# Performance work log

Measured on AMD Instinct MI355X. Metric: run time of the kernel, lower is better.

Reference implementation:

```python
import jax, jax.numpy as jnp
import numpy as np

N, E, D_IN, D_HID, D_OUT = 50000, 800000, 128, 128, 128


def setup_inputs() -> dict:
    key = jax.random.key(0)
    ks = jax.random.split(key, 10)
    x = jax.random.normal(ks[0], (N, D_IN), dtype=jnp.float32)
    edge_index = jax.random.randint(ks[1], (2, E), 0, N, dtype=jnp.int64)
    def xavier(k, fan_in, fan_out):
        lim = jnp.sqrt(6.0 / (fan_in + fan_out)).astype(jnp.float32)
        return jax.random.uniform(k, (fan_in, fan_out), jnp.float32, -lim, lim)
    return {
        "x": x,
        "edge_index": edge_index,
        "W1l": xavier(ks[2], D_IN, D_HID), "b1l": jnp.zeros((D_HID,), jnp.float32),
        "W1r": xavier(ks[3], D_IN, D_HID),
        "W2l": xavier(ks[4], D_HID, D_OUT), "b2l": jnp.zeros((D_OUT,), jnp.float32),
        "W2r": xavier(ks[5], D_HID, D_OUT),
        "Wfc": xavier(ks[6], D_OUT, 2), "bfc": jnp.zeros((2,), jnp.float32),
    }


def _mean_aggregate(x, src, dst, num_nodes):
    # gather neighbor (source) features, scatter-mean to destination nodes
    msgs = x[src]                                        # [E, D]
    summed = jax.ops.segment_sum(msgs, dst, num_segments=num_nodes)
    ones = jnp.ones((src.shape[0],), x.dtype)
    counts = jax.ops.segment_sum(ones, dst, num_segments=num_nodes)
    return summed / jnp.maximum(counts, 1.0)[:, None]


def _l2_normalize(x, eps=1e-12):
    # matches torch F.normalize(p=2, dim=-1): divide by clamp(norm, min=eps)
    norm = jnp.sqrt(jnp.sum(x * x, axis=-1, keepdims=True))
    return x / jnp.maximum(norm, eps)


def _sage_conv(x, src, dst, Wl, bl, Wr):
    agg = _mean_aggregate(x, src, dst, x.shape[0])
    out = agg @ Wl + bl + x @ Wr
    return _l2_normalize(out)


def reference(x, edge_index, W1l, b1l, W1r, W2l, b2l, W2r, Wfc, bfc):
    src, dst = edge_index[0], edge_index[1]  # PyG: row=source(j), col=target(i)
    h = _sage_conv(x, src, dst, W1l, b1l, W1r)
    h = jax.nn.relu(h)
    h = _sage_conv(h, src, dst, W2l, b2l, W2r)
    logits = h @ Wfc + bfc
    return jax.nn.softmax(logits, axis=-1)
```

## Files before the change

### kernel.cpp

```cpp
#include <hip/hip_runtime.h>

#define D 128
#define CBITS 8

typedef __attribute__((ext_vector_type(8))) short short8;
typedef __attribute__((ext_vector_type(4))) float f32x4;

__device__ __forceinline__ unsigned short f2b(float f) {
    unsigned u = __builtin_bit_cast(unsigned, f);
    u += 0x7fffu + ((u >> 16) & 1u);
    return (unsigned short)(u >> 16);
}
__device__ __forceinline__ float b2f(unsigned short b) {
    unsigned u = ((unsigned)b) << 16;
    return __builtin_bit_cast(float, u);
}


__global__ __launch_bounds__(256) void prep_kernel(
    const float* __restrict__ x, unsigned short* __restrict__ acat, int nCast, int n8,
    const float* __restrict__ W1l, const float* __restrict__ W1r,
    const float* __restrict__ W2l, const float* __restrict__ W2r,
    unsigned short* __restrict__ WT1, unsigned short* __restrict__ WT2,
    int4* __restrict__ zeroPtr, int* __restrict__ offsets, int nnodes, int E) {
    const int b = blockIdx.x;
    if (b < nCast) {
        int g = b * 256 + threadIdx.x;
        if (g < n8) {
            int row = g >> 4, chunk = g & 15;
            const float4 v0 = *reinterpret_cast<const float4*>(x + (size_t)g * 8);
            const float4 v1 = *reinterpret_cast<const float4*>(x + (size_t)g * 8 + 4);
            short8 r;
            r[0] = (short)f2b(v0.x); r[1] = (short)f2b(v0.y); r[2] = (short)f2b(v0.z); r[3] = (short)f2b(v0.w);
            r[4] = (short)f2b(v1.x); r[5] = (short)f2b(v1.y); r[6] = (short)f2b(v1.z); r[7] = (short)f2b(v1.w);
            *reinterpret_cast<short8*>(acat + (size_t)row * 256 + 128 + chunk * 8) = r;
        }
    } else if (b < nCast + 256) {
        int bb = b - nCast;
        int layer = bb >> 7;
        int j = bb & 127;
        int k = threadIdx.x;
        const float* Wl = layer ? W2l : W1l;
        const float* Wr = layer ? W2r : W1r;
        unsigned short* WT = layer ? WT2 : WT1;
        float v = (k < 128) ? Wl[k * D + j] : Wr[(k - 128) * D + j];
        WT[(size_t)j * 256 + k] = f2b(v);
    } else {
        if (threadIdx.x < 128) zeroPtr[threadIdx.x] = make_int4(0, 0, 0, 0);
        if (threadIdx.x == 0) offsets[nnodes] = E;
    }
}


__global__ __launch_bounds__(256) void bucket_count_kernel(
    const int* __restrict__ dst, int* __restrict__ bucketCnt, int E) {
    __shared__ int hist[256];
    const int t = threadIdx.x;
    hist[t] = 0;
    __syncthreads();
    const int base = blockIdx.x * 4096;
#pragma unroll
    for (int i = 0; i < 16; ++i) {
        int e = base + i * 256 + t;
        if (e < E) atomicAdd(&hist[dst[e] >> CBITS], 1);
    }
    __syncthreads();
    if (hist[t]) atomicAdd(&bucketCnt[t], hist[t]);
}

__global__ __launch_bounds__(256) void bin_coarse_kernel(
    const int* __restrict__ src, const int* __restrict__ dst,
    const int* __restrict__ bucketCnt, int* __restrict__ cursorA,
    int2* __restrict__ staging, int E) {

    __shared__ int hist[256];
    __shared__ int lcur[256];
    const int t = threadIdx.x;

    int cnt = bucketCnt[t];
    lcur[t] = cnt;
    __syncthreads();
    for (int d = 1; d < 256; d <<= 1) {
        int u = (t >= d) ? lcur[t - d] : 0;
        __syncthreads();
        lcur[t] += u;
        __syncthreads();
    }
    const int myBase = lcur[t] - cnt;
    __syncthreads();

    hist[t] = 0;
    __syncthreads();

    const int base = blockIdx.x * 4096;
    int sreg[16], dreg[16];
#pragma unroll
    for (int i = 0; i < 16; ++i) {
        int e = base + i * 256 + t;
        int s = 0, d = -1;
        if (e < E) {
            s = src[e]; d = dst[e];
            atomicAdd(&hist[d >> CBITS], 1);
        }
        sreg[i] = s; dreg[i] = d;
    }
    __syncthreads();
    {
        int h = hist[t];
        lcur[t] = myBase + (h ? atomicAdd(&cursorA[t], h) : 0);
    }
    __syncthreads();
#pragma unroll
    for (int i = 0; i < 16; ++i) {
        if (dreg[i] >= 0) {
            int p = atomicAdd(&lcur[dreg[i] >> CBITS], 1);
            staging[p] = make_int2(sreg[i], dreg[i]);
        }
    }
}

__global__ __launch_bounds__(256) void bucket_build_kernel(
    const int2* __restrict__ staging, const int* __restrict__ bucketCnt,
    int* __restrict__ offsets, int* __restrict__ csr, int nnodes) {

    __shared__ int A1[256];
    __shared__ int A2[256];
    const int t = threadIdx.x;
    const int b = blockIdx.x;

    int cnt = bucketCnt[t];
    A1[t] = cnt;
    __syncthreads();
    for (int d = 1; d < 256; d <<= 1) {
        int u = (t >= d) ? A1[t - d] : 0;
        __syncthreads();
        A1[t] += u;
        __syncthreads();
    }
    const int end  = A1[b];
    const int base = end - bucketCnt[b];
    __syncthreads();

    A1[t] = 0;
    __syncthreads();
    for (int i = base + t; i < end; i += 256)
        atomicAdd(&A1[staging[i].y & ((1 << CBITS) - 1)], 1);
    __syncthreads();
    A2[t] = A1[t];
    __syncthreads();
    for (int d = 1; d < 256; d <<= 1) {
        int u = (t >= d) ? A2[t - d] : 0;
        __syncthreads();
        A2[t] += u;
        __syncthreads();
    }
    const int excl = A2[t] - A1[t];
    const int node = (b << CBITS) + t;
    if (node < nnodes) offsets[node] = base + excl;
    __syncthreads();
    A1[t] = base + excl;
    __syncthreads();
    for (int i = base + t; i < end; i += 256) {
        int2 sd = staging[i];
        int p = atomicAdd(&A1[sd.y & ((1 << CBITS) - 1)], 1);
        csr[p] = sd.x;
    }
}


__global__ __launch_bounds__(256) void aggregate_kernel(
    const unsigned short* __restrict__ xin,
    const int* __restrict__ offsets, const int* __restrict__ csr,
    unsigned short* __restrict__ out,
    int nnodes) {
    int node = blockIdx.x * 16 + (threadIdx.x >> 4);
    int l16 = threadIdx.x & 15;
    if (node >= nnodes) return;
    int lo = offsets[node], hi = offsets[node + 1];
    float acc[8] = {0.f, 0.f, 0.f, 0.f, 0.f, 0.f, 0.f, 0.f};
    int k = lo;
    for (; k + 8 <= hi; k += 8) {
        int s[8];
        short8 v[8];
#pragma unroll
        for (int u = 0; u < 8; ++u) s[u] = csr[k + u];
#pragma unroll
        for (int u = 0; u < 8; ++u)
            v[u] = *reinterpret_cast<const short8*>(xin + (size_t)s[u] * 256 + l16 * 8);
#pragma unroll
        for (int u = 0; u < 8; ++u)
#pragma unroll
            for (int i = 0; i < 8; ++i) acc[i] += b2f((unsigned short)v[u][i]);
    }
    for (; k < hi; ++k) {
        int s = csr[k];
        const short8 v = *reinterpret_cast<const short8*>(xin + (size_t)s * 256 + l16 * 8);
#pragma unroll
        for (int i = 0; i < 8; ++i) acc[i] += b2f((unsigned short)v[i]);
    }
    float inv = 1.0f / fmaxf((float)(hi - lo), 1.0f);
    short8 r;
#pragma unroll
    for (int i = 0; i < 8; ++i) r[i] = (short)f2b(acc[i] * inv);
    *reinterpret_cast<short8*>(out + (size_t)node * 256 + l16 * 8) = r;
}


template <bool RELU, bool HEAD>
__global__ __launch_bounds__(256) void sage_mfma_kernel(
    const unsigned short* __restrict__ Acat, const unsigned short* __restrict__ WT,
    const float* __restrict__ bias, unsigned short* __restrict__ hout, int out_stride,
    const float* __restrict__ Wfc, const float* __restrict__ bfc,
    float* __restrict__ outf, int nnodes) {

    __shared__ unsigned short Blds[128 * 256];
    const int tid = threadIdx.x;

    {
        const short8* wsrc = reinterpret_cast<const short8*>(WT);
#pragma unroll
        for (int it = 0; it < 16; ++it) {
            int u = it * 256 + tid;
            int row = u >> 5, c = u & 31;
            int cs = c ^ (row & 7);
            *reinterpret_cast<short8*>(
                reinterpret_cast<char*>(Blds) + row * 512 + cs * 16) = wsrc[u];
        }
    }
    __syncthreads();

    const int w = tid >> 6, l = tid & 63;
    const int r16 = l & 15, g = l >> 4;
    const int rowbase = blockIdx.x * 128 + w * 32;

    f32x4 acc[2][8];
#pragma unroll
    for (int j = 0; j < 8; ++j) {
        float bj = bias[j * 16 + r16];
        acc[0][j] = (f32x4){bj, bj, bj, bj};
        acc[1][j] = (f32x4){bj, bj, bj, bj};
    }

    const unsigned short* ap0 = Acat + (size_t)(rowbase + r16) * 256 + g * 8;
    const unsigned short* ap1 = ap0 + 16 * 256;

#pragma unroll
    for (int ks = 0; ks < 8; ++ks) {
        const short8 a0 = *reinterpret_cast<const short8*>(ap0 + ks * 32);
        const short8 a1 = *reinterpret_cast<const short8*>(ap1 + ks * 32);
        const int cs = ((ks * 4 + g) ^ (r16 & 7)) * 16;
#pragma unroll
        for (int j = 0; j < 8; ++j) {
            const short8 b = *reinterpret_cast<const short8*>(
                reinterpret_cast<const char*>(Blds) + (j * 16 + r16) * 512 + cs);
            acc[0][j] = __builtin_amdgcn_mfma_f32_16x16x32_bf16(a0, b, acc[0][j], 0, 0, 0);
            acc[1][j] = __builtin_amdgcn_mfma_f32_16x16x32_bf16(a1, b, acc[1][j], 0, 0, 0);
        }
    }

#pragma unroll
    for (int rb = 0; rb < 2; ++rb) {
        float ss[4] = {0.f, 0.f, 0.f, 0.f};
#pragma unroll
        for (int j = 0; j < 8; ++j)
#pragma unroll
            for (int i = 0; i < 4; ++i) ss[i] += acc[rb][j][i] * acc[rb][j][i];
#pragma unroll
        for (int m = 1; m < 16; m <<= 1)
#pragma unroll
            for (int i = 0; i < 4; ++i) ss[i] += __shfl_xor(ss[i], m, 64);

        if (!HEAD) {
#pragma unroll
            for (int i = 0; i < 4; ++i) {
                int row = rowbase + rb * 16 + g * 4 + i;
                if (row >= nnodes) continue;
                float sc = 1.0f / fmaxf(sqrtf(ss[i]), 1e-12f);
#pragma unroll
                for (int j = 0; j < 8; ++j) {
                    float v = acc[rb][j][i] * sc;
                    if (RELU) v = fmaxf(v, 0.f);
                    hout[(size_t)row * out_stride + j * 16 + r16] = f2b(v);
                }
            }
        } else {
            float w0[8], w1[8];
#pragma unroll
            for (int j = 0; j < 8; ++j) {
                const float2 wv = *reinterpret_cast<const float2*>(Wfc + (j * 16 + r16) * 2);
                w0[j] = wv.x; w1[j] = wv.y;
            }
            const float b0 = bfc[0], b1 = bfc[1];
#pragma unroll
            for (int i = 0; i < 4; ++i) {
                float sc = 1.0f / fmaxf(sqrtf(ss[i]), 1e-12f);
                float l0 = 0.f, l1 = 0.f;
#pragma unroll
                for (int j = 0; j < 8; ++j) {
                    float v = acc[rb][j][i] * sc;
                    l0 = fmaf(v, w0[j], l0);
                    l1 = fmaf(v, w1[j], l1);
                }
#pragma unroll
                for (int m = 1; m < 16; m <<= 1) {
                    l0 += __shfl_xor(l0, m, 64);
                    l1 += __shfl_xor(l1, m, 64);
                }
                int row = rowbase + rb * 16 + g * 4 + i;
                if (r16 == 0 && row < nnodes) {
                    float d0 = l0 + b0, d1 = l1 + b1;
                    float mx = fmaxf(d0, d1);
                    float e0 = expf(d0 - mx), e1 = expf(d1 - mx);
                    float inv = 1.0f / (e0 + e1);
                    outf[(size_t)row * 2]     = e0 * inv;
                    outf[(size_t)row * 2 + 1] = e1 * inv;
                }
            }
        }
    }
}


extern "C" void kernel_launch(void* const* d_in, const int* in_sizes, int n_in,
                              void* d_out, int out_size, void* d_ws, size_t ws_size,
                              hipStream_t stream) {
    const float* x   = (const float*)d_in[0];
    const int*   ei  = (const int*)d_in[1];
    const float* W1l = (const float*)d_in[2];
    const float* b1l = (const float*)d_in[3];
    const float* W1r = (const float*)d_in[4];
    const float* W2l = (const float*)d_in[5];
    const float* b2l = (const float*)d_in[6];
    const float* W2r = (const float*)d_in[7];
    const float* Wfc = (const float*)d_in[8];
    const float* bfc = (const float*)d_in[9];

    const int N = in_sizes[0] / D;
    const int E = in_sizes[1] / 2;
    const int* src = ei;
    const int* dst = ei + E;
    const int NBC = (N + (1 << CBITS) - 1) >> CBITS;

    unsigned short* Acat1 = (unsigned short*)d_ws;
    unsigned short* Acat2 = Acat1 + (size_t)N * 256;
    int2* staging         = (int2*)Acat2;
    unsigned short* WT1   = Acat2 + (size_t)N * 256;
    unsigned short* WT2   = WT1 + 128 * 256;
    int* bucketCnt  = (int*)(WT2 + 128 * 256);
    int* cursorA    = bucketCnt + 256;
    int* offsets    = cursorA + 256;
    int* csr        = offsets + N + 1;

    const int nCast = (N * 16 + 255) / 256;

    prep_kernel<<<nCast + 256 + 1, 256, 0, stream>>>(
        x, Acat1, nCast, N * 16, W1l, W1r, W2l, W2r, WT1, WT2,
        (int4*)bucketCnt, offsets, N, E);

    bucket_count_kernel<<<(E + 4095) / 4096, 256, 0, stream>>>(dst, bucketCnt, E);
    bin_coarse_kernel<<<(E + 4095) / 4096, 256, 0, stream>>>(src, dst, bucketCnt, cursorA, staging, E);
    bucket_build_kernel<<<NBC, 256, 0, stream>>>(staging, bucketCnt, offsets, csr, N);

    aggregate_kernel<<<(N + 15) / 16, 256, 0, stream>>>(Acat1 + 128, offsets, csr, Acat1, N);
    sage_mfma_kernel<true, false><<<(N + 127) / 128, 256, 0, stream>>>(
        Acat1, WT1, b1l, Acat2 + 128, 256, nullptr, nullptr, nullptr, N);

    aggregate_kernel<<<(N + 15) / 16, 256, 0, stream>>>(Acat2 + 128, offsets, csr, Acat2, N);
    sage_mfma_kernel<false, true><<<(N + 127) / 128, 256, 0, stream>>>(
        Acat2, WT2, b2l, nullptr, 0, Wfc, bfc, (float*)d_out, N);
}
```

Before: 133.3 us.

## Split aggregation into feature-column slabs and pack staging edges into one int

The aggregate kernel now splits the 128 features into four 32-column slabs handled by separate block groups. Each node is served by 4 lanes instead of 16, so a block covers 64 nodes. The point is that concurrently running blocks touch a smaller slice of the gathered rows, which should help L2 locality. Staging entries are also packed into a single int (16-bit source plus 8-bit local destination) instead of int2, halving staging traffic. The packing assumes node ids fit in 16 bits, but N is 50000, so this holds only for sizes up to 65535.

```diff
diff --git a/kernel.cpp b/kernel.cpp
--- a/kernel.cpp
+++ b/kernel.cpp
@@ -71,7 +71,7 @@
 __global__ __launch_bounds__(256) void bin_coarse_kernel(
     const int* __restrict__ src, const int* __restrict__ dst,
     const int* __restrict__ bucketCnt, int* __restrict__ cursorA,
-    int2* __restrict__ staging, int E) {
+    int* __restrict__ staging, int E) {
 
     __shared__ int hist[256];
     __shared__ int lcur[256];
@@ -114,13 +114,13 @@
     for (int i = 0; i < 16; ++i) {
         if (dreg[i] >= 0) {
             int p = atomicAdd(&lcur[dreg[i] >> CBITS], 1);
-            staging[p] = make_int2(sreg[i], dreg[i]);
+            staging[p] = sreg[i] | ((dreg[i] & 255) << 16);
         }
     }
 }
 
 __global__ __launch_bounds__(256) void bucket_build_kernel(
-    const int2* __restrict__ staging, const int* __restrict__ bucketCnt,
+    const int* __restrict__ staging, const int* __restrict__ bucketCnt,
     int* __restrict__ offsets, int* __restrict__ csr, int nnodes) {
 
     __shared__ int A1[256];
@@ -144,7 +144,7 @@
     A1[t] = 0;
     __syncthreads();
     for (int i = base + t; i < end; i += 256)
-        atomicAdd(&A1[staging[i].y & ((1 << CBITS) - 1)], 1);
+        atomicAdd(&A1[(staging[i] >> 16) & 255], 1);
     __syncthreads();
     A2[t] = A1[t];
     __syncthreads();
@@ -161,9 +161,9 @@
     A1[t] = base + excl;
     __syncthreads();
     for (int i = base + t; i < end; i += 256) {
-        int2 sd = staging[i];
-        int p = atomicAdd(&A1[sd.y & ((1 << CBITS) - 1)], 1);
-        csr[p] = sd.x;
+        int p = staging[i];
+        int c = atomicAdd(&A1[(p >> 16) & 255], 1);
+        csr[c] = p & 0xFFFF;
     }
 }
 
@@ -172,10 +172,14 @@
     const unsigned short* __restrict__ xin,
     const int* __restrict__ offsets, const int* __restrict__ csr,
     unsigned short* __restrict__ out,
-    int nnodes) {
-    int node = blockIdx.x * 16 + (threadIdx.x >> 4);
-    int l16 = threadIdx.x & 15;
+    int nnodes, int nodeBlocks) {
+    const int q  = blockIdx.x / nodeBlocks;
+    const int nb = blockIdx.x - q * nodeBlocks;
+    const int node = nb * 64 + (threadIdx.x >> 2);
+    const int l4 = threadIdx.x & 3;
     if (node >= nnodes) return;
+    const int coff = q * 32 + l4 * 8;
+    const unsigned short* xq = xin + coff;
     int lo = offsets[node], hi = offsets[node + 1];
     float acc[8] = {0.f, 0.f, 0.f, 0.f, 0.f, 0.f, 0.f, 0.f};
     int k = lo;
@@ -186,7 +190,7 @@
         for (int u = 0; u < 8; ++u) s[u] = csr[k + u];
 #pragma unroll
         for (int u = 0; u < 8; ++u)
-            v[u] = *reinterpret_cast<const short8*>(xin + (size_t)s[u] * 256 + l16 * 8);
+            v[u] = *reinterpret_cast<const short8*>(xq + (size_t)s[u] * 256);
 #pragma unroll
         for (int u = 0; u < 8; ++u)
 #pragma unroll
@@ -194,7 +198,7 @@
     }
     for (; k < hi; ++k) {
         int s = csr[k];
-        const short8 v = *reinterpret_cast<const short8*>(xin + (size_t)s * 256 + l16 * 8);
+        const short8 v = *reinterpret_cast<const short8*>(xq + (size_t)s * 256);
 #pragma unroll
         for (int i = 0; i < 8; ++i) acc[i] += b2f((unsigned short)v[i]);
     }
@@ -202,7 +206,7 @@
     short8 r;
 #pragma unroll
     for (int i = 0; i < 8; ++i) r[i] = (short)f2b(acc[i] * inv);
-    *reinterpret_cast<short8*>(out + (size_t)node * 256 + l16 * 8) = r;
+    *reinterpret_cast<short8*>(out + (size_t)node * 256 + coff) = r;
 }
 
 
@@ -343,7 +347,7 @@
 
     unsigned short* Acat1 = (unsigned short*)d_ws;
     unsigned short* Acat2 = Acat1 + (size_t)N * 256;
-    int2* staging         = (int2*)Acat2;
+    int* staging          = (int*)Acat2;
     unsigned short* WT1   = Acat2 + (size_t)N * 256;
     unsigned short* WT2   = WT1 + 128 * 256;
     int* bucketCnt  = (int*)(WT2 + 128 * 256);
@@ -352,6 +356,7 @@
     int* csr        = offsets + N + 1;
 
     const int nCast = (N * 16 + 255) / 256;
+    const int nodeBlocks = (N + 63) / 64;
 
     prep_kernel<<<nCast + 256 + 1, 256, 0, stream>>>(
         x, Acat1, nCast, N * 16, W1l, W1r, W2l, W2r, WT1, WT2,
@@ -361,11 +366,11 @@
     bin_coarse_kernel<<<(E + 4095) / 4096, 256, 0, stream>>>(src, dst, bucketCnt, cursorA, staging, E);
     bucket_build_kernel<<<NBC, 256, 0, stream>>>(staging, bucketCnt, offsets, csr, N);
 
-    aggregate_kernel<<<(N + 15) / 16, 256, 0, stream>>>(Acat1 + 128, offsets, csr, Acat1, N);
+    aggregate_kernel<<<nodeBlocks * 4, 256, 0, stream>>>(Acat1 + 128, offsets, csr, Acat1, N, nodeBlocks);
     sage_mfma_kernel<true, false><<<(N + 127) / 128, 256, 0, stream>>>(
         Acat1, WT1, b1l, Acat2 + 128, 256, nullptr, nullptr, nullptr, N);
 
-    aggregate_kernel<<<(N + 15) / 16, 256, 0, stream>>>(Acat2 + 128, offsets, csr, Acat2, N);
+    aggregate_kernel<<<nodeBlocks * 4, 256, 0, stream>>>(Acat2 + 128, offsets, csr, Acat2, N, nodeBlocks);
     sage_mfma_kernel<false, true><<<(N + 127) / 128, 256, 0, stream>>>(
         Acat2, WT2, b2l, nullptr, 0, Wfc, bfc, (float*)d_out, N);
 }
```

New measurement: 156.6 us. +17.5%, slower.
